# Kernel optimization log

Measured on AMD Instinct MI355X. Metric: run time of the kernel, lower is better.

Reference implementation:

```python
import jax, jax.numpy as jnp
import numpy as np

HD = 8   # hidden_dim per node
H = 28
W = 28
B = 16


def conv2d(x, w, b):
    y = jax.lax.conv_general_dilated(x, w, (1, 1), 'SAME',
                                     dimension_numbers=('NCHW', 'OIHW', 'NCHW'))
    return y + b[None, :, None, None]


def gru_cell(x, h, td, gw, gb, cw, cb):
    # ConvGRU cell with multiplicative topdown modulation of the gate input.
    combined = jnp.concatenate([x, h], axis=1) * jax.nn.sigmoid(td)  # (B,2HD,H,W)
    r, u = jnp.split(jax.nn.sigmoid(conv2d(combined, gw, gb)), 2, axis=1)
    cand = jnp.tanh(conv2d(jnp.concatenate([x, r * h], axis=1), cw, cb))
    return (1.0 - u) * h + u * cand


def td_proj(td, w, b):
    # dynamic nn.Linear: (B, HD*H*W) -> (B, 2*HD*H*W), reshaped to feature map
    out = td.reshape(td.shape[0], -1) @ w.T + b
    return out.reshape(td.shape[0], 2 * HD, H, W)


def setup_inputs():
    key = jax.random.key(0)
    ks = jax.random.split(key, 16)
    s = 0.02
    return {
        'input_tensor': jax.random.normal(ks[0], (B, 3, 1, H, W), jnp.float32),
        'topdown_input': jax.random.normal(ks[1], (B, 2 * HD, H, W), jnp.float32),
        'input_conv_w': jax.random.normal(ks[2], (HD, 3, 3, 3), jnp.float32) * s,
        'input_conv_b': jnp.zeros((HD,), jnp.float32),
        'gates_w': jax.random.normal(ks[3], (3, 2 * HD, 2 * HD, 3, 3), jnp.float32) * s,
        'gates_b': jnp.zeros((3, 2 * HD), jnp.float32),
        'can_w': jax.random.normal(ks[4], (3, HD, 2 * HD, 3, 3), jnp.float32) * s,
        'can_b': jnp.zeros((3, HD), jnp.float32),
        'td_w0': jax.random.normal(ks[5], (2 * HD * H * W, HD * H * W), jnp.float32) * s,
        'td_b0': jnp.zeros((2 * HD * H * W,), jnp.float32),
        'td_w1': jax.random.normal(ks[6], (2 * HD * H * W, HD * H * W), jnp.float32) * s,
        'td_b1': jnp.zeros((2 * HD * H * W,), jnp.float32),
        'fc1_w': jax.random.normal(ks[7], (100, HD * H * W), jnp.float32) * s,
        'fc1_b': jnp.zeros((100,), jnp.float32),
        'fc2_w': jax.random.normal(ks[8], (10, 100), jnp.float32) * s,
        'fc2_b': jnp.zeros((10,), jnp.float32),
    }


def reference(input_tensor, topdown_input, input_conv_w, input_conv_b,
              gates_w, gates_b, can_w, can_b,
              td_w0, td_b0, td_w1, td_b1, fc1_w, fc1_b, fc2_w, fc2_b):
    b = input_tensor.shape[0]
    z = jnp.zeros((b, HD, H, W), input_tensor.dtype)
    prev = [z, z, z]
    cur = [z, z, z]
    # input layout (b,c,t,h,w); permute+index picks frame t=0
    cur_input = conv2d(input_tensor[:, :, 0], input_conv_w, input_conv_b)
    for step in range(2):  # reps=2, max(seq_len, max_rank)=1 -> 2 graph sweeps
        # node 0 (input node): bottomup = input conv; feedback from node 1 (0.6)
        td0 = td_proj(0.6 * prev[1], td_w0, td_b0)
        cur[0] = gru_cell(cur_input, prev[0], td0,
                          gates_w[0], gates_b[0], can_w[0], can_b[0])
        # node 1: feedforward from node 0 (0.8); feedback from node 2 (0.5)
        td1 = td_proj(0.5 * prev[2], td_w1, td_b1)
        cur[1] = gru_cell(0.8 * prev[0], prev[1], td1,
                          gates_w[1], gates_b[1], can_w[1], can_b[1])
        # node 2 (output node): feedforward from node 1 (0.7); external topdown
        cur[2] = gru_cell(0.7 * prev[1], prev[2], topdown_input,
                          gates_w[2], gates_b[2], can_w[2], can_b[2])
        # faithful to torch: hidden_state_prev = hidden_state_cur aliases the
        # list, so sweeps after the first see in-sweep node updates
        prev = cur
    pred = jax.nn.relu(cur[2].reshape(b, -1)) @ fc1_w.T + fc1_b
    pred = jax.nn.relu(pred) @ fc2_w.T + fc2_b
    return pred
```

## Files before the change

### kernel.cpp

```cpp
#include <hip/hip_runtime.h>
#include <cstddef>

#define HD 8
#define C2 16
#define HH 28
#define WW 28
#define BB 16
#define SP (HH*WW)
#define FEAT (HD*SP)
#define FEAT2 (C2*SP)

#define TILE_ROWS 2
#define NT (HH/TILE_ROWS)
#define NBLK (BB*NT)
#define NTHR 768

#define X0_R 18
#define H00_R 14
#define H10_R 10
#define H11_R 6

__device__ __forceinline__ float sigf(float x) { return 1.0f / (1.0f + expf(-x)); }

union F4 { float4 v; float f[4]; };

struct SM {
    float gwt[C2*9][16];
    float cwt[C2*9][8];
    float gb[C2];
    float cb[HD];
    float hc1[HD];
    float hc2[HD];
    float comb[C2][18][32];
    union {
        float rh[HD][16][32];
        float s_in[3][TILE_ROWS+18][32];
    } u;
    float su[HD][14][32];
    float x0e[HD][X0_R][32];
    float h00e[HD][H00_R][32];
    float h10e[HD][H10_R][32];
    float h11e[HD][H11_R][32];
};

__device__ __forceinline__ void gbar(unsigned* arrive, unsigned* release,
                                     int blk, unsigned ep) {
    __syncthreads();
    __threadfence();
    if (threadIdx.x == 0)
        __hip_atomic_store(&arrive[(size_t)blk * 16], ep,
                           __ATOMIC_RELEASE, __HIP_MEMORY_SCOPE_AGENT);
    if (blk == 0) {
        int t = threadIdx.x;
        if (t < NBLK) {
            while (__hip_atomic_load(&arrive[(size_t)t * 16],
                                     __ATOMIC_RELAXED, __HIP_MEMORY_SCOPE_AGENT) < ep)
                __builtin_amdgcn_s_sleep(32);
        }
        __syncthreads();
        if (t < NBLK)
            __hip_atomic_store(&release[(size_t)t * 16], ep,
                               __ATOMIC_RELEASE, __HIP_MEMORY_SCOPE_AGENT);
    } else {
        if (threadIdx.x == 0) {
            while (__hip_atomic_load(&release[(size_t)blk * 16],
                                     __ATOMIC_RELAXED, __HIP_MEMORY_SCOPE_AGENT) < ep)
                __builtin_amdgcn_s_sleep(32);
        }
    }
    __threadfence();
    __syncthreads();
}

__device__ __forceinline__ void stage_node(SM& sm, int tid, int n,
                           const float* gates_w, const float* gates_b,
                           const float* can_w, const float* can_b) {
    for (int i = tid; i < C2*C2*9; i += NTHR) {
        int oc = i & 15, r = i >> 4;
        sm.gwt[r][oc] = gates_w[n*C2*C2*9 + oc*C2*9 + r];
    }
    for (int i = tid; i < C2*9*8; i += NTHR) {
        int oc = i & 7, r = i >> 3;
        sm.cwt[r][oc] = can_w[n*HD*C2*9 + oc*C2*9 + r];
    }
    if (tid < C2) sm.gb[tid] = gates_b[n*C2 + tid];
    if (tid < HD) sm.cb[tid] = can_b[n*HD + tid];
}

template<int XS>
__device__ __forceinline__ const float* xrow(SM& sm, int c, int ridx) {
    if constexpr (XS == 0) return &sm.x0e[c][ridx][0];
    else if constexpr (XS == 1) return &sm.h10e[c][ridx][0];
    else return &sm.h11e[c][ridx][0];
}

template<int M, int XS, int HS, int OS>
__device__ void cell(SM& sm, int tid, int bi, int r0, float xs,
                     const float* __restrict__ td, float* __restrict__ h12g) {
    constexpr int R1 = M + 4, R2 = M + 2;
    constexpr int NIC = (HS == 0) ? HD : C2;
    const int ca    = (OS == 0) ? r0-6 : (OS == 1) ? r0-4 : (OS == 2) ? r0-2 : r0;
    const int xbase = (XS == 0) ? r0-8 : (XS == 1) ? r0-4 : r0-2;
    const int hbase = r0 - 6;

    for (int i = tid; i < NIC*R1*8; i += NTHR) {
        int ci4 = i & 7, rr = (i >> 3) % R1, c = i / (8*R1);
        int row = ca - 2 + rr;
        F4 v; v.f[0] = v.f[1] = v.f[2] = v.f[3] = 0.0f;
        if (row >= 0 && row < HH) {
            F4 base;
            if (c < HD) {
                base.v = *(const float4*)(xrow<XS>(sm, c, row - xbase) + ci4*4);
                #pragma unroll
                for (int e = 0; e < 4; ++e) base.f[e] *= xs;
            } else {
                if constexpr (HS == 1)
                    base.v = *(const float4*)(&sm.h00e[c-HD][row - hbase][ci4*4]);
                else if constexpr (HS == 2) {
                    float h = sm.hc1[c-HD];
                    base.f[0] = base.f[1] = base.f[2] = base.f[3] = h;
                } else {
                    float h = sm.hc2[c-HD];
                    base.f[0] = base.f[1] = base.f[2] = base.f[3] = h;
                }
            }
            const float* tdr = td + c*SP + row*WW;
            #pragma unroll
            for (int e = 0; e < 4; ++e) {
                int col = ci4*4 + e - 2;
                if (col >= 0 && col < WW)
                    v.f[e] = base.f[e] * sigf(tdr[col]);
            }
        }
        *(float4*)&sm.comb[c][rr][ci4*4] = v.v;
    }
    __syncthreads();

    constexpr int itemsU = 2*M*32;
    if constexpr (HS != 0) {
        constexpr int itemsB = 2*R2*32;
        for (int i = tid; i < itemsB + itemsU; i += NTHR) {
            if (i < itemsB) {
                int ci = i & 31, rr = (i >> 5) % R2, g = i / (32*R2);
                int row = ca - 1 + rr, col = ci - 2;
                bool inb = (col >= 0 && col < WW && row >= 0 && row < HH);
                float a0 = sm.gb[g*4+0], a1 = sm.gb[g*4+1],
                      a2 = sm.gb[g*4+2], a3 = sm.gb[g*4+3];
                if (inb) {
                    #pragma unroll 2
                    for (int ic = 0; ic < C2; ++ic) {
                        const float* wb = &sm.gwt[ic*9][g*4];
                        #pragma unroll
                        for (int dy = 0; dy < 3; ++dy)
                            #pragma unroll
                            for (int dx = 0; dx < 3; ++dx) {
                                float cvv = sm.comb[ic][rr+dy][ci-1+dx];
                                F4 w; w.v = *(const float4*)(wb + (dy*3+dx)*16);
                                a0 += cvv*w.f[0]; a1 += cvv*w.f[1];
                                a2 += cvv*w.f[2]; a3 += cvv*w.f[3];
                            }
                    }
                }
                float av[4] = {a0, a1, a2, a3};
                #pragma unroll
                for (int o = 0; o < 4; ++o) {
                    int c = g*4 + o;
                    float v = 0.0f;
                    if (inb) {
                        float hv;
                        if constexpr (HS == 1) hv = sm.h00e[c][row - hbase][ci];
                        else if constexpr (HS == 2) hv = sm.hc1[c];
                        else hv = sm.hc2[c];
                        v = sigf(av[o]) * hv;
                    }
                    sm.u.rh[c][rr][ci] = v;
                }
            } else {
                int j = i - itemsB;
                int ci = j & 31, rr = (j >> 5) % M, g = j / (32*M);
                int row = ca + rr, col = ci - 2;
                bool inb = (col >= 0 && col < WW && row >= 0 && row < HH);
                float a0 = sm.gb[HD+g*4+0], a1 = sm.gb[HD+g*4+1],
                      a2 = sm.gb[HD+g*4+2], a3 = sm.gb[HD+g*4+3];
                if (inb) {
                    #pragma unroll 2
                    for (int ic = 0; ic < C2; ++ic) {
                        const float* wb = &sm.gwt[ic*9][HD + g*4];
                        #pragma unroll
                        for (int dy = 0; dy < 3; ++dy)
                            #pragma unroll
                            for (int dx = 0; dx < 3; ++dx) {
                                float cvv = sm.comb[ic][rr+1+dy][ci-1+dx];
                                F4 w; w.v = *(const float4*)(wb + (dy*3+dx)*16);
                                a0 += cvv*w.f[0]; a1 += cvv*w.f[1];
                                a2 += cvv*w.f[2]; a3 += cvv*w.f[3];
                            }
                    }
                }
                float av[4] = {a0, a1, a2, a3};
                #pragma unroll
                for (int o = 0; o < 4; ++o)
                    sm.su[g*4+o][rr][ci] = sigf(av[o]);
            }
        }
    } else {
        for (int i = tid; i < itemsU; i += NTHR) {
            int ci = i & 31, rr = (i >> 5) % M, g = i / (32*M);
            int row = ca + rr, col = ci - 2;
            bool inb = (col >= 0 && col < WW && row >= 0 && row < HH);
            float a0 = sm.gb[HD+g*4+0], a1 = sm.gb[HD+g*4+1],
                  a2 = sm.gb[HD+g*4+2], a3 = sm.gb[HD+g*4+3];
            if (inb) {
                #pragma unroll 2
                for (int ic = 0; ic < HD; ++ic) {
                    const float* wb = &sm.gwt[ic*9][HD + g*4];
                    #pragma unroll
                    for (int dy = 0; dy < 3; ++dy)
                        #pragma unroll
                        for (int dx = 0; dx < 3; ++dx) {
                            float cvv = sm.comb[ic][rr+1+dy][ci-1+dx];
                            F4 w; w.v = *(const float4*)(wb + (dy*3+dx)*16);
                            a0 += cvv*w.f[0]; a1 += cvv*w.f[1];
                            a2 += cvv*w.f[2]; a3 += cvv*w.f[3];
                        }
                }
            }
            float av[4] = {a0, a1, a2, a3};
            #pragma unroll
            for (int o = 0; o < 4; ++o)
                sm.su[g*4+o][rr][ci] = sigf(av[o]);
        }
    }
    __syncthreads();

    for (int i = tid; i < 2*M*32; i += NTHR) {
        int ci = i & 31, rr = (i >> 5) % M, g = i / (32*M);
        int row = ca + rr, col = ci - 2;
        bool inb = (col >= 0 && col < WW && row >= 0 && row < HH);
        float a0 = sm.cb[g*4+0], a1 = sm.cb[g*4+1],
              a2 = sm.cb[g*4+2], a3 = sm.cb[g*4+3];
        if (inb) {
            #pragma unroll 2
            for (int ic = 0; ic < HD; ++ic) {
                const float* wb = &sm.cwt[ic*9][g*4];
                #pragma unroll
                for (int dy = 0; dy < 3; ++dy) {
                    const float* xr = xrow<XS>(sm, ic, (row - 1 + dy) - xbase);
                    #pragma unroll
                    for (int dx = 0; dx < 3; ++dx) {
                        float civ = xs * xr[ci-1+dx];
                        F4 w; w.v = *(const float4*)(wb + (dy*3+dx)*8);
                        a0 += civ*w.f[0]; a1 += civ*w.f[1];
                        a2 += civ*w.f[2]; a3 += civ*w.f[3];
                    }
                }
            }
            if constexpr (HS != 0) {
                #pragma unroll 2
                for (int ic = HD; ic < C2; ++ic) {
                    const float* wb = &sm.cwt[ic*9][g*4];
                    #pragma unroll
                    for (int dy = 0; dy < 3; ++dy)
                        #pragma unroll
                        for (int dx = 0; dx < 3; ++dx) {
                            float civ = sm.u.rh[ic-HD][rr+dy][ci-1+dx];
                            F4 w; w.v = *(const float4*)(wb + (dy*3+dx)*8);
                            a0 += civ*w.f[0]; a1 += civ*w.f[1];
                            a2 += civ*w.f[2]; a3 += civ*w.f[3];
                        }
                }
            }
        }
        float av[4] = {a0, a1, a2, a3};
        #pragma unroll
        for (int o = 0; o < 4; ++o) {
            int c = g*4 + o;
            float outv = 0.0f;
            if (inb) {
                float uu = sm.su[c][rr][ci];
                float cand = tanhf(av[o]);
                float hv;
                if constexpr (HS == 1) hv = sm.h00e[c][row - hbase][ci];
                else if constexpr (HS == 2) hv = sm.hc1[c];
                else if constexpr (HS == 3) hv = sm.hc2[c];
                else hv = 0.0f;
                outv = (1.0f - uu) * hv + uu * cand;
            }
            if constexpr (OS == 0) sm.h00e[c][row - (r0-6)][ci] = outv;
            else if constexpr (OS == 1) sm.h10e[c][row - (r0-4)][ci] = outv;
            else if constexpr (OS == 2) sm.h11e[c][row - (r0-2)][ci] = outv;
            else {
                if (inb)
                    h12g[((size_t)bi*HD + c)*SP + row*WW + col] = outv;
            }
        }
    }
    __syncthreads();
}

__global__ void init_kernel(unsigned* arrive, unsigned* release) {
    int t = threadIdx.x;
    for (int i = t; i < NBLK*16; i += 256) { arrive[i] = 0u; release[i] = 0u; }
}

__global__ __launch_bounds__(NTHR, 3)
void mega_kernel(const float* __restrict__ input_tensor, const float* __restrict__ topdown,
                 const float* __restrict__ icw, const float* __restrict__ icb,
                 const float* __restrict__ gates_w, const float* __restrict__ gates_b,
                 const float* __restrict__ can_w, const float* __restrict__ can_b,
                 const float* __restrict__ td_w0, const float* __restrict__ td_b0,
                 const float* __restrict__ td_w1, const float* __restrict__ td_b1,
                 float* __restrict__ h12g,
                 float* __restrict__ td0c, float* __restrict__ td1c,
                 unsigned* arrive, unsigned* release)
{
    const int tid = threadIdx.x;
    const int blk = blockIdx.x;
    const int bi  = blk / NT;
    const int r0  = (blk % NT) * TILE_ROWS;

    __shared__ SM sm;

    if (tid < HD) {
        sm.hc1[tid] = sigf(gates_b[1*C2 + HD + tid]) * tanhf(can_b[1*HD + tid]);
        sm.hc2[tid] = sigf(gates_b[2*C2 + HD + tid]) * tanhf(can_b[2*HD + tid]);
    }
    bool f0 = false, f1 = false;
    for (int c = 0; c < HD; ++c) {
        f0 |= (sigf(gates_b[1*C2 + HD + c]) * tanhf(can_b[1*HD + c])) != 0.0f;
        f1 |= (sigf(gates_b[2*C2 + HD + c]) * tanhf(can_b[2*HD + c])) != 0.0f;
    }

    for (int i = tid; i < 3*(TILE_ROWS+18)*32; i += NTHR) {
        int ci = i & 31, rr = (i >> 5) % (TILE_ROWS+18), c = i / (32*(TILE_ROWS+18));
        int row = r0 - 9 + rr, col = ci - 2;
        float v = 0.0f;
        if (row >= 0 && row < HH && col >= 0 && col < WW)
            v = input_tensor[((size_t)bi*3 + c)*SP + row*WW + col];
        sm.u.s_in[c][rr][ci] = v;
    }
    for (int i = tid; i < 3*9*8; i += NTHR) {
        int oc = i & 7, r = i >> 3;
        sm.gwt[r][oc] = icw[oc*27 + r];
    }
    if (tid < HD) sm.cb[tid] = icb[tid];
    __syncthreads();

    for (int i = tid; i < X0_R*32; i += NTHR) {
        int ci = i & 31, rr = i >> 5;
        int row = r0 - 8 + rr, col = ci - 2;
        float acc[8];
        if (row >= 0 && row < HH && col >= 0 && col < WW) {
            #pragma unroll
            for (int o = 0; o < 8; ++o) acc[o] = sm.cb[o];
            for (int ic = 0; ic < 3; ++ic)
                #pragma unroll
                for (int dy = 0; dy < 3; ++dy)
                    #pragma unroll
                    for (int dx = 0; dx < 3; ++dx) {
                        float a = sm.u.s_in[ic][rr+dy][ci-1+dx];
                        F4 w0, w1;
                        w0.v = *(const float4*)&sm.gwt[ic*9+dy*3+dx][0];
                        w1.v = *(const float4*)&sm.gwt[ic*9+dy*3+dx][4];
                        acc[0] += a*w0.f[0]; acc[1] += a*w0.f[1];
                        acc[2] += a*w0.f[2]; acc[3] += a*w0.f[3];
                        acc[4] += a*w1.f[0]; acc[5] += a*w1.f[1];
                        acc[6] += a*w1.f[2]; acc[7] += a*w1.f[3];
                    }
        } else {
            #pragma unroll
            for (int o = 0; o < 8; ++o) acc[o] = 0.0f;
        }
        #pragma unroll
        for (int o = 0; o < 8; ++o) sm.x0e[o][rr][ci] = acc[o];
    }
    __syncthreads();

    stage_node(sm, tid, 0, gates_w, gates_b, can_w, can_b);
    cell<14, 0, 0, 0>(sm, tid, bi, r0, 1.0f, td_b0, nullptr);

    if (f0 | f1) {
        if (f0) {
            for (int j = blk*NTHR + tid; j < FEAT2; j += NBLK*NTHR) {
                float s = td_b0[j];
                const float* wr = td_w0 + (size_t)j * FEAT;
                for (int c = 0; c < HD; ++c) {
                    float hcv = sm.hc1[c];
                    if (hcv != 0.0f) {
                        float ss = 0.0f;
                        for (int p = 0; p < SP; ++p) ss += wr[c*SP + p];
                        s += 0.6f * hcv * ss;
                    }
                }
                td0c[j] = s;
            }
        }
        if (f1) {
            for (int j = blk*NTHR + tid; j < FEAT2; j += NBLK*NTHR) {
                float s = td_b1[j];
                const float* wr = td_w1 + (size_t)j * FEAT;
                for (int c = 0; c < HD; ++c) {
                    float hcv = sm.hc2[c];
                    if (hcv != 0.0f) {
                        float ss = 0.0f;
                        for (int p = 0; p < SP; ++p) ss += wr[c*SP + p];
                        s += 0.5f * hcv * ss;
                    }
                }
                td1c[j] = s;
            }
        }
        gbar(arrive, release, blk, 1u);
    }
    const float* td0v = f0 ? td0c : td_b0;
    const float* td1v = f1 ? td1c : td_b1;

    cell<10, 0, 1, 1>(sm, tid, bi, r0, 1.0f, td0v, nullptr);

    stage_node(sm, tid, 1, gates_w, gates_b, can_w, can_b);
    cell<6, 1, 2, 2>(sm, tid, bi, r0, 0.8f, td1v, nullptr);

    stage_node(sm, tid, 2, gates_w, gates_b, can_w, can_b);
    cell<2, 2, 3, 3>(sm, tid, bi, r0, 0.7f, topdown + (size_t)bi*FEAT2, h12g);
}

__global__ __launch_bounds__(512)
void fc1_kernel(const float* __restrict__ in, const float* __restrict__ w,
                const float* __restrict__ b, float* __restrict__ out) {
    int j    = blockIdx.x;
    int wave = threadIdx.x >> 6;
    int lane = threadIdx.x & 63;
    float acc[2] = {0.f, 0.f};
    const float* wr = w + (size_t)j * FEAT;
    for (int k = lane; k < FEAT; k += 64) {
        float wv = wr[k];
        #pragma unroll
        for (int q = 0; q < 2; ++q) {
            float v = in[(size_t)(wave*2+q)*FEAT + k];
            acc[q] += fmaxf(v, 0.0f) * wv;
        }
    }
    #pragma unroll
    for (int off = 32; off > 0; off >>= 1)
        #pragma unroll
        for (int q = 0; q < 2; ++q)
            acc[q] += __shfl_down(acc[q], off);
    if (lane == 0) {
        #pragma unroll
        for (int q = 0; q < 2; ++q)
            out[(size_t)(wave*2+q)*100 + j] = acc[q] + b[j];
    }
}

__global__ __launch_bounds__(256)
void fc2_kernel(const float* __restrict__ p1, const float* __restrict__ w,
                const float* __restrict__ b, float* __restrict__ out) {
    int t = threadIdx.x;
    if (t >= BB*10) return;
    int bi = t / 10, j = t % 10;
    float acc = b[j];
    for (int k = 0; k < 100; ++k)
        acc += fmaxf(p1[bi*100 + k], 0.0f) * w[j*100 + k];
    out[bi*10 + j] = acc;
}

extern "C" void kernel_launch(void* const* d_in, const int* in_sizes, int n_in,
                              void* d_out, int out_size, void* d_ws, size_t ws_size,
                              hipStream_t stream) {
    const float* input_tensor = (const float*)d_in[0];
    const float* topdown      = (const float*)d_in[1];
    const float* icw  = (const float*)d_in[2];
    const float* icb  = (const float*)d_in[3];
    const float* gates_w = (const float*)d_in[4];
    const float* gates_b = (const float*)d_in[5];
    const float* can_w   = (const float*)d_in[6];
    const float* can_b   = (const float*)d_in[7];
    const float* td_w0 = (const float*)d_in[8];
    const float* td_b0 = (const float*)d_in[9];
    const float* td_w1 = (const float*)d_in[10];
    const float* td_b1 = (const float*)d_in[11];
    const float* fc1_w = (const float*)d_in[12];
    const float* fc1_b = (const float*)d_in[13];
    const float* fc2_w = (const float*)d_in[14];
    const float* fc2_b = (const float*)d_in[15];
    float* out = (float*)d_out;

    float* ws   = (float*)d_ws;
    float* h12g = ws;
    float* p1   = h12g + BB*HD*SP;
    float* td0c = p1 + BB*100;
    float* td1c = td0c + FEAT2;
    unsigned* arrive  = (unsigned*)((char*)d_ws + (16u << 20));
    unsigned* release = arrive + NBLK*16;

    init_kernel<<<1, 256, 0, stream>>>(arrive, release);
    mega_kernel<<<NBLK, NTHR, 0, stream>>>(
        input_tensor, topdown, icw, icb, gates_w, gates_b, can_w, can_b,
        td_w0, td_b0, td_w1, td_b1,
        h12g, td0c, td1c, arrive, release);
    fc1_kernel<<<100, 512, 0, stream>>>(h12g, fc1_w, fc1_b, p1);
    fc2_kernel<<<1, 256, 0, stream>>>(p1, fc2_w, fc2_b, out);
}
```

Before: 101.6 us.

## Fuse fc1 partial products into mega kernel and merge fc reduction with fc2

Each mega-kernel block now computes fc1 partial dot products over its own two-row tile of the final hidden state and writes per-block partials. A single tail kernel sums the partials across tiles, adds the bias, applies relu and runs fc2. This removes one kernel launch and the separate full pass over h12g, in exchange for extra work at the end of the mega kernel with strided fc1_w reads. It relies on the block having just written its h12g tile and reading it back after a block-level sync inside cell.

```diff
diff --git a/kernel.cpp b/kernel.cpp
--- a/kernel.cpp
+++ b/kernel.cpp
@@ -310,7 +310,8 @@
                  const float* __restrict__ can_w, const float* __restrict__ can_b,
                  const float* __restrict__ td_w0, const float* __restrict__ td_b0,
                  const float* __restrict__ td_w1, const float* __restrict__ td_b1,
-                 float* __restrict__ h12g,
+                 const float* __restrict__ fc1_w,
+                 float* __restrict__ h12g, float* __restrict__ p1p,
                  float* __restrict__ td0c, float* __restrict__ td1c,
                  unsigned* arrive, unsigned* release)
 {
@@ -422,46 +423,53 @@
 
     stage_node(sm, tid, 2, gates_w, gates_b, can_w, can_b);
     cell<2, 2, 3, 3>(sm, tid, bi, r0, 0.7f, topdown + (size_t)bi*FEAT2, h12g);
-}
-
-__global__ __launch_bounds__(512)
-void fc1_kernel(const float* __restrict__ in, const float* __restrict__ w,
-                const float* __restrict__ b, float* __restrict__ out) {
-    int j    = blockIdx.x;
-    int wave = threadIdx.x >> 6;
-    int lane = threadIdx.x & 63;
-    float acc[2] = {0.f, 0.f};
-    const float* wr = w + (size_t)j * FEAT;
-    for (int k = lane; k < FEAT; k += 64) {
-        float wv = wr[k];
-        #pragma unroll
-        for (int q = 0; q < 2; ++q) {
-            float v = in[(size_t)(wave*2+q)*FEAT + k];
-            acc[q] += fmaxf(v, 0.0f) * wv;
-        }
-    }
-    #pragma unroll
-    for (int off = 32; off > 0; off >>= 1)
-        #pragma unroll
-        for (int q = 0; q < 2; ++q)
-            acc[q] += __shfl_down(acc[q], off);
-    if (lane == 0) {
-        #pragma unroll
-        for (int q = 0; q < 2; ++q)
-            out[(size_t)(wave*2+q)*100 + j] = acc[q] + b[j];
-    }
-}
-
-__global__ __launch_bounds__(256)
-void fc2_kernel(const float* __restrict__ p1, const float* __restrict__ w,
-                const float* __restrict__ b, float* __restrict__ out) {
+
+    {
+        float* scratch = &sm.comb[0][0][0];
+        if (tid < 400) {
+            int j = tid >> 2, p = tid & 3;
+            float acc = 0.0f;
+            for (int s = 0; s < 112; ++s) {
+                int kl  = p*112 + s;
+                int c   = kl / 56;
+                int rem = kl % 56;
+                int rr  = rem / 28, col = rem % 28;
+                int k   = c*SP + (r0 + rr)*WW + col;
+                float v = h12g[(size_t)bi*FEAT + k];
+                acc += fmaxf(v, 0.0f) * fc1_w[(size_t)j*FEAT + k];
+            }
+            scratch[j*4 + p] = acc;
+        }
+        __syncthreads();
+        if (tid < 100) {
+            float s = scratch[tid*4+0] + scratch[tid*4+1]
+                    + scratch[tid*4+2] + scratch[tid*4+3];
+            p1p[(size_t)blk*100 + tid] = s;
+        }
+    }
+}
+
+__global__ __launch_bounds__(1024)
+void fc_tail_kernel(const float* __restrict__ p1p, const float* __restrict__ fc1_b,
+                    const float* __restrict__ fc2_w, const float* __restrict__ fc2_b,
+                    float* __restrict__ out) {
+    __shared__ float p1[BB*100];
     int t = threadIdx.x;
-    if (t >= BB*10) return;
-    int bi = t / 10, j = t % 10;
-    float acc = b[j];
-    for (int k = 0; k < 100; ++k)
-        acc += fmaxf(p1[bi*100 + k], 0.0f) * w[j*100 + k];
-    out[bi*10 + j] = acc;
+    for (int idx = t; idx < BB*100; idx += 1024) {
+        int b = idx / 100, j = idx % 100;
+        float s = fc1_b[j];
+        for (int q = 0; q < NT; ++q)
+            s += p1p[(size_t)(b*NT + q)*100 + j];
+        p1[idx] = fmaxf(s, 0.0f);
+    }
+    __syncthreads();
+    if (t < BB*10) {
+        int b = t / 10, j = t % 10;
+        float acc = fc2_b[j];
+        for (int k = 0; k < 100; ++k)
+            acc += p1[b*100 + k] * fc2_w[j*100 + k];
+        out[b*10 + j] = acc;
+    }
 }
 
 extern "C" void kernel_launch(void* const* d_in, const int* in_sizes, int n_in,
@@ -487,8 +495,8 @@
 
     float* ws   = (float*)d_ws;
     float* h12g = ws;
-    float* p1   = h12g + BB*HD*SP;
-    float* td0c = p1 + BB*100;
+    float* p1p  = h12g + BB*HD*SP;
+    float* td0c = p1p + NBLK*100;
     float* td1c = td0c + FEAT2;
     unsigned* arrive  = (unsigned*)((char*)d_ws + (16u << 20));
     unsigned* release = arrive + NBLK*16;
@@ -496,8 +504,7 @@
     init_kernel<<<1, 256, 0, stream>>>(arrive, release);
     mega_kernel<<<NBLK, NTHR, 0, stream>>>(
         input_tensor, topdown, icw, icb, gates_w, gates_b, can_w, can_b,
-        td_w0, td_b0, td_w1, td_b1,
-        h12g, td0c, td1c, arrive, release);
-    fc1_kernel<<<100, 512, 0, stream>>>(h12g, fc1_w, fc1_b, p1);
-    fc2_kernel<<<1, 256, 0, stream>>>(p1, fc2_w, fc2_b, out);
-}
+        td_w0, td_b0, td_w1, td_b1, fc1_w,
+        h12g, p1p, td0c, td1c, arrive, release);
+    fc_tail_kernel<<<1, 1024, 0, stream>>>(p1p, fc1_b, fc2_w, fc2_b, out);
+}
```

Result: faster. 94.53 us (-6.9%).
